# Kernel tuning notes

Hardware: AMD Instinct MI355X
Metric: run time of the kernel (lower is better)

## Reference

```python
import jax, jax.numpy as jnp
import numpy as np

EPS = 1e-6
N_HEADS = 16


def _stable_softmax(x):
    # max subtracted with stop_gradient (torch .detach()), clamp to [-50, 50], eps in denom
    x_max = jax.lax.stop_gradient(jnp.max(x, axis=-1, keepdims=True))
    exp_x = jnp.exp(jnp.clip(x - x_max, -50.0, 50.0))
    return exp_x / (jnp.sum(exp_x, axis=-1, keepdims=True) + EPS)


def setup_inputs() -> dict:
    key = jax.random.key(0)
    k1, k2, k3 = jax.random.split(key, 3)
    B, S, D = 2, 2048, 1024
    x = jax.random.normal(k1, (B, S, D), dtype=jnp.float32)
    Wqkv = jax.random.normal(k2, (3 * D, D), dtype=jnp.float32) * 0.02
    Wout = jax.random.normal(k3, (D, D), dtype=jnp.float32) * (0.02 / np.sqrt(2))
    return {"x": x, "Wqkv": Wqkv, "Wout": Wout}


def reference(x, Wqkv, Wout):
    B, S, D = x.shape
    H = N_HEADS
    Dh = D // H
    scale = 1.0 / np.sqrt(Dh)
    # qkv projection (torch Linear: x @ W.T), split into q,k,v -> (B,H,S,Dh)
    qkv = (x @ Wqkv.T).reshape(B, S, 3, H, Dh)
    qkv = jnp.transpose(qkv, (2, 0, 3, 1, 4))
    q, k, v = qkv[0], qkv[1], qkv[2]
    # chunked attention is mathematically identical to full attention here
    scores = jnp.einsum('bhqd,bhkd->bhqk', q, k) * scale
    attn = _stable_softmax(scores)
    out = jnp.einsum('bhqk,bhkd->bhqd', attn, v)  # (B,H,S,Dh)
    out = jnp.transpose(out, (0, 2, 1, 3)).reshape(B, S, D)
    return out @ Wout.T
```

## Files before the change

### kernel.cpp

```cpp
#include <hip/hip_runtime.h>
#include <hip/hip_bf16.h>
#include <stdint.h>

#define S_LEN   2048
#define D_MODEL 1024
#define NH      16
#define DH      64
#define BATCH   2
#define TOKENS  (BATCH * S_LEN)

typedef __bf16 bf16;
typedef __bf16 bf16x8 __attribute__((ext_vector_type(8)));
typedef __bf16 b16x4  __attribute__((ext_vector_type(4)));
typedef float  f32x4  __attribute__((ext_vector_type(4)));
typedef float  f32x16 __attribute__((ext_vector_type(16)));
typedef unsigned int uint32;

__device__ __forceinline__ void async_lds16(const void* g, void* l) {
  __builtin_amdgcn_global_load_lds((__attribute__((address_space(1))) void*)g,
                                   (__attribute__((address_space(3))) void*)l,
                                   16, 0, 0);
}

__global__ __launch_bounds__(256) void convert2_kernel(
    const float* __restrict__ s0, bf16* __restrict__ d0, int n0,
    const float* __restrict__ s1, bf16* __restrict__ d1, int n1) {
  int i = blockIdx.x * 256 + threadIdx.x;
  const float* s;
  bf16* d;
  if (i < n0) {
    s = s0 + (size_t)i * 8; d = d0 + (size_t)i * 8;
  } else {
    i -= n0;
    if (i >= n1) return;
    s = s1 + (size_t)i * 8; d = d1 + (size_t)i * 8;
  }
  const f32x4 a = *(const f32x4*)s;
  const f32x4 b = *(const f32x4*)(s + 4);
  bf16x8 o;
#pragma unroll
  for (int j = 0; j < 4; j++) { o[j] = (bf16)a[j]; o[j + 4] = (bf16)b[j]; }
  *(bf16x8*)d = o;
}

#define BM 128
#define BN 128
#define BK 32

#define GEMM_CORE(APTR, BPTR, KDIM)                                              \
  __shared__ __align__(16) bf16 As[BM * BK];                                     \
  __shared__ __align__(16) bf16 Bs[BN * BK];                                     \
  const int tid  = threadIdx.x;                                                  \
  const int wave = tid >> 6, lane = tid & 63;                                    \
  const int quad = lane >> 4, l16 = lane & 15;                                   \
  const int m0 = blockIdx.y * BM;                                                \
  const int n0 = blockIdx.x * BN;                                                \
  const int wm = (wave >> 1) * 64, wn = (wave & 1) * 64;                         \
  f32x4 acc[4][4] = {};                                                          \
  const int c0 = tid, c1 = tid + 256;                                            \
  for (int k0 = 0; k0 < (KDIM); k0 += BK) {                                      \
    async_lds16((APTR) + (size_t)(m0 + (c0 >> 2)) * (KDIM) + k0 + (c0 & 3) * 8,  \
                As + c0 * 8);                                                    \
    async_lds16((APTR) + (size_t)(m0 + (c1 >> 2)) * (KDIM) + k0 + (c1 & 3) * 8,  \
                As + c1 * 8);                                                    \
    async_lds16((BPTR) + (size_t)(n0 + (c0 >> 2)) * (KDIM) + k0 + (c0 & 3) * 8,  \
                Bs + c0 * 8);                                                    \
    async_lds16((BPTR) + (size_t)(n0 + (c1 >> 2)) * (KDIM) + k0 + (c1 & 3) * 8,  \
                Bs + c1 * 8);                                                    \
    __syncthreads();                                                             \
    bf16x8 af[4], bfr[4];                                                        \
    _Pragma("unroll") for (int i = 0; i < 4; i++)                                \
        af[i] = *(const bf16x8*)(As + (wm + i * 16 + l16) * BK + quad * 8);      \
    _Pragma("unroll") for (int j = 0; j < 4; j++)                                \
        bfr[j] = *(const bf16x8*)(Bs + (wn + j * 16 + l16) * BK + quad * 8);     \
    _Pragma("unroll") for (int i = 0; i < 4; i++)                                \
      _Pragma("unroll") for (int j = 0; j < 4; j++)                              \
        acc[i][j] = __builtin_amdgcn_mfma_f32_16x16x32_bf16(af[i], bfr[j],       \
                                                            acc[i][j], 0, 0, 0); \
    __syncthreads();                                                             \
  }

__global__ __launch_bounds__(256) void gemm_qkv_kernel(
    const bf16* __restrict__ X, const bf16* __restrict__ W,
    bf16* __restrict__ Qo, bf16* __restrict__ Ko, bf16* __restrict__ VTo) {
  GEMM_CORE(X, W, D_MODEL)
  const int t = n0 >> 10;
#pragma unroll
  for (int i = 0; i < 4; i++) {
    const int rowb = m0 + wm + i * 16 + quad * 4;
    const int b = rowb >> 11, s0 = rowb & 2047;
#pragma unroll
    for (int j = 0; j < 4; j++) {
      const int col = n0 + wn + j * 16 + l16;
      const int h = (col >> 6) & 15, d = col & 63;
      if (t == 2) {
        b16x4 v4;
#pragma unroll
        for (int r = 0; r < 4; r++) v4[r] = (bf16)acc[i][j][r];
        *(b16x4*)(VTo + ((size_t)(b * NH + h) * DH + d) * S_LEN + s0) = v4;
      } else {
#pragma unroll
        for (int r = 0; r < 4; r++) {
          const float v = acc[i][j][r];
          if (t == 0)
            Qo[((size_t)(b * NH + h) * S_LEN + s0 + r) * DH + d] = (bf16)(v * 0.125f);
          else
            Ko[((size_t)(b * NH + h) * S_LEN + s0 + r) * DH + d] = (bf16)v;
        }
      }
    }
  }
}

__global__ __launch_bounds__(256) void gemm_out_kernel(
    const bf16* __restrict__ A, const float* __restrict__ WF,
    float* __restrict__ Out) {
  __shared__ __align__(16) bf16 As[BM * BK];
  __shared__ __align__(16) bf16 Bs[BN * BK];
  const int tid  = threadIdx.x;
  const int wave = tid >> 6, lane = tid & 63;
  const int quad = lane >> 4, l16 = lane & 15;
  const int m0 = blockIdx.y * BM;
  const int n0 = blockIdx.x * BN;
  const int wm = (wave >> 1) * 64, wn = (wave & 1) * 64;
  f32x4 acc[4][4] = {};
  const int c0 = tid, c1 = tid + 256;
  for (int k0 = 0; k0 < D_MODEL; k0 += BK) {
    async_lds16(A + (size_t)(m0 + (c0 >> 2)) * D_MODEL + k0 + (c0 & 3) * 8,
                As + c0 * 8);
    async_lds16(A + (size_t)(m0 + (c1 >> 2)) * D_MODEL + k0 + (c1 & 3) * 8,
                As + c1 * 8);
    {
      const float* wp0 = WF + (size_t)(n0 + (c0 >> 2)) * D_MODEL + k0 + (c0 & 3) * 8;
      const float* wp1 = WF + (size_t)(n0 + (c1 >> 2)) * D_MODEL + k0 + (c1 & 3) * 8;
      const f32x4 a0 = *(const f32x4*)wp0, b0 = *(const f32x4*)(wp0 + 4);
      const f32x4 a1 = *(const f32x4*)wp1, b1 = *(const f32x4*)(wp1 + 4);
      bf16x8 v0, v1;
#pragma unroll
      for (int j = 0; j < 4; j++) {
        v0[j] = (bf16)a0[j]; v0[j + 4] = (bf16)b0[j];
        v1[j] = (bf16)a1[j]; v1[j + 4] = (bf16)b1[j];
      }
      *(bf16x8*)(Bs + c0 * 8) = v0;
      *(bf16x8*)(Bs + c1 * 8) = v1;
    }
    __syncthreads();
    bf16x8 af[4], bfr[4];
#pragma unroll
    for (int i = 0; i < 4; i++)
      af[i] = *(const bf16x8*)(As + (wm + i * 16 + l16) * BK + quad * 8);
#pragma unroll
    for (int j = 0; j < 4; j++)
      bfr[j] = *(const bf16x8*)(Bs + (wn + j * 16 + l16) * BK + quad * 8);
#pragma unroll
    for (int i = 0; i < 4; i++)
#pragma unroll
      for (int j = 0; j < 4; j++)
        acc[i][j] = __builtin_amdgcn_mfma_f32_16x16x32_bf16(af[i], bfr[j],
                                                            acc[i][j], 0, 0, 0);
    __syncthreads();
  }
#pragma unroll
  for (int i = 0; i < 4; i++) {
    const int rowb = m0 + wm + i * 16 + quad * 4;
#pragma unroll
    for (int j = 0; j < 4; j++) {
      const int col = n0 + wn + j * 16 + l16;
#pragma unroll
      for (int r = 0; r < 4; r++)
        Out[(size_t)(rowb + r) * D_MODEL + col] = acc[i][j][r];
    }
  }
}

__global__ __launch_bounds__(512, 2) void attn_kernel(
    const bf16* __restrict__ Q, const bf16* __restrict__ K,
    const bf16* __restrict__ VT, bf16* __restrict__ AO) {
  __shared__ __align__(16) bf16 smem[2][2][2 * 64 * 64];

  const int tid  = threadIdx.x;
  const int lane = tid & 63;
  const int wave = tid >> 6;
  const int g    = wave >> 2;
  const int qw   = wave & 3;
  const int l31  = lane & 31;
  const int hi   = lane >> 5;
  const int sw   = l31 & 7;

  const int bid = (blockIdx.x & 7) * 32 + (blockIdx.x >> 3);
  const int qb  = bid & 7;
  const int bh  = bid >> 3;

  const bf16* qp = Q  + ((size_t)bh * S_LEN + qb * 256 + qw * 64 + l31) * DH;
  const bf16* kp = K  + (size_t)bh * S_LEN * DH;
  const bf16* vp = VT + (size_t)bh * DH * S_LEN;

  bf16x8 qf0[4], qf1[4];
#pragma unroll
  for (int dk = 0; dk < 4; dk++) {
    qf0[dk] = *(const bf16x8*)(qp + dk * 16 + hi * 8);
    qf1[dk] = *(const bf16x8*)(qp + 32 * DH + dk * 16 + hi * 8);
  }

  const int gtid = tid & 255;
  const int cid0 = gtid, cid1 = gtid + 256;
  const int r0 = cid0 >> 3, c0 = (cid0 & 7) ^ (r0 & 7);
  const int r1 = cid1 >> 3, c1 = (cid1 & 7) ^ (r1 & 7);
  const bf16* ka0 = kp + (size_t)(g * 64 + r0) * DH + c0 * 8;
  const bf16* ka1 = kp + (size_t)(g * 64 + r1) * DH + c1 * 8;
  const bf16* va0 = vp + (size_t)r0 * S_LEN + g * 64 + c0 * 8;
  const bf16* va1 = vp + (size_t)r1 * S_LEN + g * 64 + c1 * 8;
  const int ld0 = cid0 * 8, ld1 = cid1 * 8;

  f32x16 oT0[2] = {}, oT1[2] = {};
  float lsum0 = 0.f, lsum1 = 0.f;

  bf16* sg = &smem[g][0][0];

#define STAGE(B)                                                                 \
  {                                                                              \
    bf16* s = sg + (B) * (2 * 64 * 64);                                          \
    async_lds16(ka0, s + ld0);                                                   \
    async_lds16(ka1, s + ld1);                                                   \
    async_lds16(va0, s + 4096 + ld0);                                            \
    async_lds16(va1, s + 4096 + ld1);                                            \
    ka0 += 8192; ka1 += 8192; va0 += 128; va1 += 128;                            \
  }

  STAGE(0)

#pragma unroll 2
  for (int t = 0; t < 16; t++) {
    const int cur = t & 1;
    asm volatile("s_waitcnt vmcnt(0)" ::: "memory");
    __builtin_amdgcn_s_barrier();
    if (t < 15) {
      STAGE(cur ^ 1)
    }

    const bf16* sb = sg + cur * (2 * 64 * 64);

    bf16x8 vfr[8];
#pragma unroll
    for (int dt = 0; dt < 2; dt++)
#pragma unroll
      for (int ks = 0; ks < 4; ks++)
        vfr[dt * 4 + ks] = *(const bf16x8*)(sb + 4096 + (dt * 32 + l31) * 64 +
                                            (((ks * 2 + hi) ^ sw) * 8));

    f32x16 st0[2] = {}, st1[2] = {};
    __builtin_amdgcn_s_setprio(1);
#pragma unroll
    for (int kt = 0; kt < 2; kt++)
#pragma unroll
      for (int dk = 0; dk < 4; dk++) {
        const bf16x8 kf = *(const bf16x8*)(sb + (kt * 32 + l31) * 64 +
                                           (((dk * 2 + hi) ^ sw) * 8));
        st0[kt] = __builtin_amdgcn_mfma_f32_32x32x16_bf16(kf, qf0[dk], st0[kt], 0, 0, 0);
        st1[kt] = __builtin_amdgcn_mfma_f32_32x32x16_bf16(kf, qf1[dk], st1[kt], 0, 0, 0);
      }
    __builtin_amdgcn_s_setprio(0);

#pragma unroll
    for (int kt = 0; kt < 2; kt++)
#pragma unroll
      for (int hk = 0; hk < 2; hk++) {
        const int ks = kt * 2 + hk;
        float e0[8], e1[8];
#pragma unroll
        for (int r = 0; r < 8; r++) e0[r] = __expf(st0[kt][hk * 8 + r]);
#pragma unroll
        for (int r = 0; r < 8; r++) e1[r] = __expf(st1[kt][hk * 8 + r]);
        lsum0 += ((e0[0] + e0[1]) + (e0[2] + e0[3])) + ((e0[4] + e0[5]) + (e0[6] + e0[7]));
        lsum1 += ((e1[0] + e1[1]) + (e1[2] + e1[3])) + ((e1[4] + e1[5]) + (e1[6] + e1[7]));
        uint32 p00, p01, p02, p03, p10, p11, p12, p13;
        asm("v_cvt_pk_bf16_f32 %0, %1, %2" : "=v"(p00) : "v"(e0[0]), "v"(e0[1]));
        asm("v_cvt_pk_bf16_f32 %0, %1, %2" : "=v"(p01) : "v"(e0[2]), "v"(e0[3]));
        asm("v_cvt_pk_bf16_f32 %0, %1, %2" : "=v"(p02) : "v"(e0[4]), "v"(e0[5]));
        asm("v_cvt_pk_bf16_f32 %0, %1, %2" : "=v"(p03) : "v"(e0[6]), "v"(e0[7]));
        asm("v_cvt_pk_bf16_f32 %0, %1, %2" : "=v"(p10) : "v"(e1[0]), "v"(e1[1]));
        asm("v_cvt_pk_bf16_f32 %0, %1, %2" : "=v"(p11) : "v"(e1[2]), "v"(e1[3]));
        asm("v_cvt_pk_bf16_f32 %0, %1, %2" : "=v"(p12) : "v"(e1[4]), "v"(e1[5]));
        asm("v_cvt_pk_bf16_f32 %0, %1, %2" : "=v"(p13) : "v"(e1[6]), "v"(e1[7]));
        asm("v_permlane32_swap_b32 %0, %1" : "+v"(p00), "+v"(p02));
        asm("v_permlane32_swap_b32 %0, %1" : "+v"(p01), "+v"(p03));
        asm("v_permlane32_swap_b32 %0, %1" : "+v"(p10), "+v"(p12));
        asm("v_permlane32_swap_b32 %0, %1" : "+v"(p11), "+v"(p13));
        union { uint32 u[4]; bf16x8 v; } pf0, pf1;
        pf0.u[0] = p00; pf0.u[1] = p01; pf0.u[2] = p02; pf0.u[3] = p03;
        pf1.u[0] = p10; pf1.u[1] = p11; pf1.u[2] = p12; pf1.u[3] = p13;
        __builtin_amdgcn_s_setprio(1);
#pragma unroll
        for (int dt = 0; dt < 2; dt++) {
          oT0[dt] = __builtin_amdgcn_mfma_f32_32x32x16_bf16(vfr[dt * 4 + ks], pf0.v,
                                                            oT0[dt], 0, 0, 0);
          oT1[dt] = __builtin_amdgcn_mfma_f32_32x32x16_bf16(vfr[dt * 4 + ks], pf1.v,
                                                            oT1[dt], 0, 0, 0);
        }
        __builtin_amdgcn_s_setprio(0);
      }
  }
#undef STAGE

  __syncthreads();

  lsum0 += __shfl_xor(lsum0, 32);
  lsum1 += __shfl_xor(lsum1, 32);

  float* mO = (float*)&smem[0][0][0];
  float* mL = mO + 256 * 32;
  const int mrow = qw * 64 + lane;

  if (g == 1) {
#pragma unroll
    for (int j = 0; j < 8; j++) {
      const int dt = j >> 2, rb = (j & 3) * 4;
      f32x4 c = { oT0[dt][rb], oT0[dt][rb + 1], oT0[dt][rb + 2], oT0[dt][rb + 3] };
      *(f32x4*)((char*)mO + mrow * 128 + ((j ^ (lane & 7)) * 16)) = c;
    }
    mL[mrow] = lsum0;
  }
  __syncthreads();
  if (g == 0) {
#pragma unroll
    for (int j = 0; j < 8; j++) {
      const int dt = j >> 2, rb = (j & 3) * 4;
      const f32x4 c = *(const f32x4*)((char*)mO + mrow * 128 + ((j ^ (lane & 7)) * 16));
#pragma unroll
      for (int rr = 0; rr < 4; rr++) oT0[dt][rb + rr] += c[rr];
    }
    lsum0 += mL[mrow];
  }
  __syncthreads();
  if (g == 1) {
#pragma unroll
    for (int j = 0; j < 8; j++) {
      const int dt = j >> 2, rb = (j & 3) * 4;
      f32x4 c = { oT1[dt][rb], oT1[dt][rb + 1], oT1[dt][rb + 2], oT1[dt][rb + 3] };
      *(f32x4*)((char*)mO + mrow * 128 + ((j ^ (lane & 7)) * 16)) = c;
    }
    mL[mrow] = lsum1;
  }
  __syncthreads();
  if (g == 0) {
#pragma unroll
    for (int j = 0; j < 8; j++) {
      const int dt = j >> 2, rb = (j & 3) * 4;
      const f32x4 c = *(const f32x4*)((char*)mO + mrow * 128 + ((j ^ (lane & 7)) * 16));
#pragma unroll
      for (int rr = 0; rr < 4; rr++) oT1[dt][rb + rr] += c[rr];
    }
    lsum1 += mL[mrow];

    const float inv0 = 1.0f / (lsum0 + 1e-6f);
    const float inv1 = 1.0f / (lsum1 + 1e-6f);
    const int b = bh >> 4, h = bh & 15;
    const int srow = qb * 256 + qw * 64 + l31;
    const size_t base0 = (size_t)(b * S_LEN + srow) * D_MODEL + h * DH;
    const size_t base1 = base0 + (size_t)32 * D_MODEL;
#pragma unroll
    for (int dt = 0; dt < 2; dt++)
#pragma unroll
      for (int rg = 0; rg < 4; rg++) {
        b16x4 o4;
#pragma unroll
        for (int rr = 0; rr < 4; rr++) o4[rr] = (bf16)(oT0[dt][rg * 4 + rr] * inv0);
        *(b16x4*)(AO + base0 + dt * 32 + rg * 8 + hi * 4) = o4;
      }
#pragma unroll
    for (int dt = 0; dt < 2; dt++)
#pragma unroll
      for (int rg = 0; rg < 4; rg++) {
        b16x4 o4;
#pragma unroll
        for (int rr = 0; rr < 4; rr++) o4[rr] = (bf16)(oT1[dt][rg * 4 + rr] * inv1);
        *(b16x4*)(AO + base1 + dt * 32 + rg * 8 + hi * 4) = o4;
      }
  }
}

extern "C" void kernel_launch(void* const* d_in, const int* in_sizes, int n_in,
                              void* d_out, int out_size, void* d_ws, size_t ws_size,
                              hipStream_t stream) {
  const float* x    = (const float*)d_in[0];
  const float* wqkv = (const float*)d_in[1];
  const float* wout = (const float*)d_in[2];
  float* out = (float*)d_out;

  bf16* Q  = (bf16*)d_ws;
  bf16* K  = Q  + (size_t)TOKENS * D_MODEL;
  bf16* VT = K  + (size_t)TOKENS * D_MODEL;
  bf16* xb = VT + (size_t)TOKENS * D_MODEL;
  bf16* AO = xb;
  bf16* wqkvb = (bf16*)d_out;

  const int nx = TOKENS * D_MODEL / 8;
  const int nw = 3 * D_MODEL * D_MODEL / 8;
  convert2_kernel<<<dim3((nx + nw) / 256), dim3(256), 0, stream>>>(
      x, xb, nx, wqkv, wqkvb, nw);

  gemm_qkv_kernel<<<dim3(3 * D_MODEL / BN, TOKENS / BM), dim3(256), 0, stream>>>(
      xb, wqkvb, Q, K, VT);

  attn_kernel<<<dim3(BATCH * NH * (S_LEN / 256)), dim3(512), 0, stream>>>(Q, K, VT, AO);

  gemm_out_kernel<<<dim3(D_MODEL / BN, TOKENS / BM), dim3(256), 0, stream>>>(
      AO, wout, out);
}
```

Baseline: 187.4 us.

## Pre-convert Wout to bf16 and shrink output GEMM tile to 64x128

After: 179.8 us. 4.0% less time.

```diff
diff --git a/kernel.cpp b/kernel.cpp
--- a/kernel.cpp
+++ b/kernel.cpp
@@ -112,48 +112,39 @@
   }
 }
 
+#define BM2 64
+#define BN2 128
+
 __global__ __launch_bounds__(256) void gemm_out_kernel(
-    const bf16* __restrict__ A, const float* __restrict__ WF,
+    const bf16* __restrict__ A, const bf16* __restrict__ W,
     float* __restrict__ Out) {
-  __shared__ __align__(16) bf16 As[BM * BK];
-  __shared__ __align__(16) bf16 Bs[BN * BK];
+  __shared__ __align__(16) bf16 As[BM2 * BK];
+  __shared__ __align__(16) bf16 Bs[BN2 * BK];
   const int tid  = threadIdx.x;
   const int wave = tid >> 6, lane = tid & 63;
   const int quad = lane >> 4, l16 = lane & 15;
-  const int m0 = blockIdx.y * BM;
-  const int n0 = blockIdx.x * BN;
-  const int wm = (wave >> 1) * 64, wn = (wave & 1) * 64;
-  f32x4 acc[4][4] = {};
+  const int m0 = blockIdx.y * BM2;
+  const int n0 = blockIdx.x * BN2;
+  const int wm = (wave >> 1) * 32, wn = (wave & 1) * 64;
+  f32x4 acc[2][4] = {};
   const int c0 = tid, c1 = tid + 256;
   for (int k0 = 0; k0 < D_MODEL; k0 += BK) {
     async_lds16(A + (size_t)(m0 + (c0 >> 2)) * D_MODEL + k0 + (c0 & 3) * 8,
                 As + c0 * 8);
-    async_lds16(A + (size_t)(m0 + (c1 >> 2)) * D_MODEL + k0 + (c1 & 3) * 8,
-                As + c1 * 8);
-    {
-      const float* wp0 = WF + (size_t)(n0 + (c0 >> 2)) * D_MODEL + k0 + (c0 & 3) * 8;
-      const float* wp1 = WF + (size_t)(n0 + (c1 >> 2)) * D_MODEL + k0 + (c1 & 3) * 8;
-      const f32x4 a0 = *(const f32x4*)wp0, b0 = *(const f32x4*)(wp0 + 4);
-      const f32x4 a1 = *(const f32x4*)wp1, b1 = *(const f32x4*)(wp1 + 4);
-      bf16x8 v0, v1;
-#pragma unroll
-      for (int j = 0; j < 4; j++) {
-        v0[j] = (bf16)a0[j]; v0[j + 4] = (bf16)b0[j];
-        v1[j] = (bf16)a1[j]; v1[j + 4] = (bf16)b1[j];
-      }
-      *(bf16x8*)(Bs + c0 * 8) = v0;
-      *(bf16x8*)(Bs + c1 * 8) = v1;
-    }
+    async_lds16(W + (size_t)(n0 + (c0 >> 2)) * D_MODEL + k0 + (c0 & 3) * 8,
+                Bs + c0 * 8);
+    async_lds16(W + (size_t)(n0 + (c1 >> 2)) * D_MODEL + k0 + (c1 & 3) * 8,
+                Bs + c1 * 8);
     __syncthreads();
-    bf16x8 af[4], bfr[4];
-#pragma unroll
-    for (int i = 0; i < 4; i++)
+    bf16x8 af[2], bfr[4];
+#pragma unroll
+    for (int i = 0; i < 2; i++)
       af[i] = *(const bf16x8*)(As + (wm + i * 16 + l16) * BK + quad * 8);
 #pragma unroll
     for (int j = 0; j < 4; j++)
       bfr[j] = *(const bf16x8*)(Bs + (wn + j * 16 + l16) * BK + quad * 8);
 #pragma unroll
-    for (int i = 0; i < 4; i++)
+    for (int i = 0; i < 2; i++)
 #pragma unroll
       for (int j = 0; j < 4; j++)
         acc[i][j] = __builtin_amdgcn_mfma_f32_16x16x32_bf16(af[i], bfr[j],
@@ -161,7 +152,7 @@
     __syncthreads();
   }
 #pragma unroll
-  for (int i = 0; i < 4; i++) {
+  for (int i = 0; i < 2; i++) {
     const int rowb = m0 + wm + i * 16 + quad * 4;
 #pragma unroll
     for (int j = 0; j < 4; j++) {
@@ -393,9 +384,11 @@
   bf16* xb = VT + (size_t)TOKENS * D_MODEL;
   bf16* AO = xb;
   bf16* wqkvb = (bf16*)d_out;
+  bf16* woutb = Q;
 
   const int nx = TOKENS * D_MODEL / 8;
   const int nw = 3 * D_MODEL * D_MODEL / 8;
+  const int no = D_MODEL * D_MODEL / 8;
   convert2_kernel<<<dim3((nx + nw) / 256), dim3(256), 0, stream>>>(
       x, xb, nx, wqkv, wqkvb, nw);
 
@@ -404,6 +397,9 @@
 
   attn_kernel<<<dim3(BATCH * NH * (S_LEN / 256)), dim3(512), 0, stream>>>(Q, K, VT, AO);
 
-  gemm_out_kernel<<<dim3(D_MODEL / BN, TOKENS / BM), dim3(256), 0, stream>>>(
-      AO, wout, out);
-}
+  convert2_kernel<<<dim3(no / 256), dim3(256), 0, stream>>>(
+      wout, woutb, no, wout, woutb, 0);
+
+  gemm_out_kernel<<<dim3(D_MODEL / BN2, TOKENS / BM2), dim3(256), 0, stream>>>(
+      AO, woutb, out);
+}
```
